# Performance work log

Measured on AMD Instinct MI355X. Metric: run time of the kernel, lower is better.

## Reference

```python
import jax, jax.numpy as jnp
import numpy as np
import math

N_HEADS = 4          # h2_dim*n_heads must equal g_dim for the stacked layers
H2_DIM = 32
G_DIM = 128
N_REL = 4
N_LAYERS = 2
PAST_W, FUT_W, PERIODIC = 5, 5, [15]
LN_EPS = 1e-5
BN_EPS = 1e-5


def _build_edges(d):
    ei, et = [], []
    for t in range(d):
        ei.append([t, t]); et.append(0)                      # self-loop
        for off in range(1, PAST_W + 1):
            if t - off >= 0:
                ei.append([t, t - off]); et.append(1)        # past
        for off in range(1, FUT_W + 1):
            if t + off < d:
                ei.append([t, t + off]); et.append(2)        # future
        for off in PERIODIC:
            if t + off < d:
                ei.append([t, t + off]); et.append(3)        # periodic fwd
            if t - off >= 0:
                ei.append([t, t - off]); et.append(3)        # periodic bwd
    return np.array(ei, dtype=np.int64).T, np.array(et, dtype=np.int64)


def setup_inputs() -> dict:
    key = jax.random.key(0)
    b, d, h, w, c = 4, 2048, 8, 8, 192
    ks = jax.random.split(key, 24)
    s = 0.05
    ei, et = _build_edges(d)
    inp = {
        'x': jax.random.normal(ks[0], (b, d, h, w, c), dtype=jnp.float32),
        'edge_index': jnp.asarray(ei),
        'edge_type': jnp.asarray(et),
        'fe_fc_w': jax.random.normal(ks[1], (c, G_DIM), dtype=jnp.float32) * s,
        'fe_fc_b': jnp.zeros((G_DIM,), jnp.float32),
        'fe_ln_g': jnp.ones((G_DIM,), jnp.float32),
        'fe_ln_b': jnp.zeros((G_DIM,), jnp.float32),
        'w_rel': jax.random.normal(ks[2], (N_LAYERS, N_REL, G_DIM, G_DIM), dtype=jnp.float32) * s,
        'w_root': jax.random.normal(ks[3], (N_LAYERS, G_DIM, G_DIM), dtype=jnp.float32) * s,
        'rgcn_b': jnp.zeros((N_LAYERS, G_DIM), jnp.float32),
        'wq': jax.random.normal(ks[4], (N_LAYERS, G_DIM, N_HEADS * H2_DIM), dtype=jnp.float32) * s,
        'bq': jnp.zeros((N_LAYERS, N_HEADS * H2_DIM), jnp.float32),
        'wk': jax.random.normal(ks[5], (N_LAYERS, G_DIM, N_HEADS * H2_DIM), dtype=jnp.float32) * s,
        'bk': jnp.zeros((N_LAYERS, N_HEADS * H2_DIM), jnp.float32),
        'wv': jax.random.normal(ks[6], (N_LAYERS, G_DIM, N_HEADS * H2_DIM), dtype=jnp.float32) * s,
        'bv': jnp.zeros((N_LAYERS, N_HEADS * H2_DIM), jnp.float32),
        'wskip': jax.random.normal(ks[7], (N_LAYERS, G_DIM, N_HEADS * H2_DIM), dtype=jnp.float32) * s,
        'bskip': jnp.zeros((N_LAYERS, N_HEADS * H2_DIM), jnp.float32),
        'bn_g': jnp.ones((N_LAYERS, N_HEADS * H2_DIM), jnp.float32),
        'bn_b': jnp.zeros((N_LAYERS, N_HEADS * H2_DIM), jnp.float32),
    }
    return inp


def _forward(x, edge_index, edge_type, fe_fc_w, fe_fc_b, fe_ln_g, fe_ln_b,
             w_rel, w_root, rgcn_b, wq, bq, wk, bk, wv, bv, wskip, bskip, bn_g, bn_b):
    d = x.shape[1]
    src, dst = edge_index[0], edge_index[1]
    rel_masks = [(edge_type == r).astype(jnp.float32) for r in range(N_REL)]
    inv_sqrt_c = 1.0 / math.sqrt(H2_DIM)

    def graph_fwd(xi):  # xi: [d,h,w,c]
        feat = xi.mean(axis=(1, 2))                         # adaptive avg pool -> [d,c]
        hfe = feat @ fe_fc_w + fe_fc_b                      # [d,g]
        mu = hfe.mean(-1, keepdims=True)
        var = ((hfe - mu) ** 2).mean(-1, keepdims=True)
        nf = (hfe - mu) / jnp.sqrt(var + LN_EPS) * fe_ln_g + fe_ln_b

        for l in range(N_LAYERS):
            # ---- RGCNConv (mean aggregation per relation + root) ----
            out = nf @ w_root[l] + rgcn_b[l]
            for r in range(N_REL):
                m = rel_masks[r]
                xr = nf @ w_rel[l, r]                       # [d,g]
                msg = xr[src] * m[:, None]                  # [E,g]
                s = jax.ops.segment_sum(msg, dst, num_segments=d)
                cnt = jax.ops.segment_sum(m, dst, num_segments=d)
                out = out + s / jnp.maximum(cnt, 1.0)[:, None]
            nf1 = out
            # ---- TransformerConv (per-head edge attention) ----
            q = (nf1 @ wq[l] + bq[l]).reshape(d, N_HEADS, H2_DIM)
            k = (nf1 @ wk[l] + bk[l]).reshape(d, N_HEADS, H2_DIM)
            v = (nf1 @ wv[l] + bv[l]).reshape(d, N_HEADS, H2_DIM)
            logits = (q[dst] * k[src]).sum(-1) * inv_sqrt_c  # [E,H]
            mx = jax.ops.segment_max(logits, dst, num_segments=d)
            a = jnp.exp(logits - mx[dst])
            denom = jax.ops.segment_sum(a, dst, num_segments=d)
            alpha = a / denom[dst]                           # softmax over incoming edges
            agg = jax.ops.segment_sum(alpha[:, :, None] * v[src], dst, num_segments=d)
            out2 = agg.reshape(d, N_HEADS * H2_DIM) + nf1 @ wskip[l] + bskip[l]
            # ---- BatchNorm1d (training-mode batch stats over nodes) ----
            bmu = out2.mean(0)
            bvar = ((out2 - bmu) ** 2).mean(0)
            out2 = (out2 - bmu) / jnp.sqrt(bvar + BN_EPS) * bn_g[l] + bn_b[l]
            nf = jax.nn.leaky_relu(out2, 0.01)
        return nf

    return jax.vmap(graph_fwd)(x)                           # [b,d,g]


def reference(x, edge_index, edge_type, fe_fc_w, fe_fc_b, fe_ln_g, fe_ln_b,
              w_rel, w_root, rgcn_b, wq, bq, wk, bk, wv, bv, wskip, bskip, bn_g, bn_b):
    return _forward(x, edge_index, edge_type, fe_fc_w, fe_fc_b, fe_ln_g, fe_ln_b,
                    w_rel, w_root, rgcn_b, wq, bq, wk, bk, wv, bv, wskip, bskip, bn_g, bn_b)
```

## Files before the change

### kernel.cpp

```cpp
#include <hip/hip_runtime.h>
#include <hip/hip_bf16.h>

#define B_ 4
#define D_ 2048
#define HWS 64
#define C_ 192
#define G_ 128
#define NODES (B_*D_)
#define R_ 16
#define HALO_ROWS 48

typedef short bf8_t  __attribute__((ext_vector_type(8)));
typedef float f32x4_t __attribute__((ext_vector_type(4)));
typedef unsigned short us4_t __attribute__((ext_vector_type(4)));

__device__ inline unsigned short f2bf(float f) {
    unsigned int u = __builtin_bit_cast(unsigned int, f);
    unsigned int r = (u + 0x7fffu + ((u >> 16) & 1u)) >> 16;
    return (unsigned short)r;
}
__device__ inline float bf2f(unsigned short h) {
    unsigned int u = ((unsigned int)h) << 16;
    return __builtin_bit_cast(float, u);
}

struct WconvArgs {
    const float* src[16];
    const float* add[16];
};
__global__ __launch_bounds__(256) void wconv_kernel(WconvArgs a, unsigned short* __restrict__ dst)
{
    int m = blockIdx.y;
    int idx = blockIdx.x * 256 + threadIdx.x;
    int n = idx >> 7;
    int k = idx & 127;
    float v = a.src[m][k * G_ + n];
    if (a.add[m]) v += a.add[m][k * G_ + n];
    dst[(size_t)m * 16384 + idx] = f2bf(v);
}

__global__ __launch_bounds__(192) void pool_fc_ln_kernel(
    const float* __restrict__ x, const float* __restrict__ W,
    const float* __restrict__ bias, const float* __restrict__ gam,
    const float* __restrict__ bet, unsigned short* __restrict__ nf)
{
    int u = blockIdx.x;
    int tid = threadIdx.x;
    __shared__ float feat[C_];
    __shared__ float4 red4[4][48];
    __shared__ float red[4];
    __shared__ float stats[2];

    const float4* xb4 = (const float4*)(x + (size_t)u * (HWS * C_));
    int cg = tid % 48;
    int rg = tid / 48;
    float4 a = make_float4(0.f, 0.f, 0.f, 0.f);
    #pragma unroll
    for (int s = 0; s < HWS; s += 4) {
        float4 v = xb4[(size_t)(s + rg) * 48 + cg];
        a.x += v.x; a.y += v.y; a.z += v.z; a.w += v.w;
    }
    red4[rg][cg] = a;
    __syncthreads();
    if (rg == 0) {
        float4 b0 = red4[0][cg], b1 = red4[1][cg], b2 = red4[2][cg], b3 = red4[3][cg];
        feat[cg * 4 + 0] = (b0.x + b1.x + b2.x + b3.x) * (1.0f / HWS);
        feat[cg * 4 + 1] = (b0.y + b1.y + b2.y + b3.y) * (1.0f / HWS);
        feat[cg * 4 + 2] = (b0.z + b1.z + b2.z + b3.z) * (1.0f / HWS);
        feat[cg * 4 + 3] = (b0.w + b1.w + b2.w + b3.w) * (1.0f / HWS);
    }
    __syncthreads();

    float h = 0.f;
    if (tid < G_) {
        h = bias[tid];
        #pragma unroll 4
        for (int c = 0; c < C_; ++c) h += feat[c] * W[c * G_ + tid];
    }
    float s1 = (tid < G_) ? h : 0.f;
    float s2 = (tid < G_) ? h * h : 0.f;
    #pragma unroll
    for (int off = 32; off >= 1; off >>= 1) {
        s1 += __shfl_xor(s1, off, 64);
        s2 += __shfl_xor(s2, off, 64);
    }
    int wid = tid >> 6;
    if ((tid & 63) == 0 && wid < 2) { red[wid] = s1; red[2 + wid] = s2; }
    __syncthreads();
    if (tid == 0) {
        float S = red[0] + red[1];
        float SS = red[2] + red[3];
        float mu = S / G_;
        float var = SS / G_ - mu * mu;
        stats[0] = mu;
        stats[1] = 1.0f / sqrtf(var + 1e-5f);
    }
    __syncthreads();
    if (tid < G_) {
        float v = (h - stats[0]) * stats[1] * gam[tid] + bet[tid];
        nf[(size_t)u * G_ + tid] = f2bf(v);
    }
}

template <bool BNIN>
__global__ __launch_bounds__(256) void rgcn_fused_kernel(
    const unsigned short* __restrict__ nf, const float* __restrict__ xin,
    const float* __restrict__ partials, const float* __restrict__ gam,
    const float* __restrict__ bet,
    const unsigned short* __restrict__ wt,
    const float* __restrict__ rb,
    unsigned short* __restrict__ out)
{
    __shared__ char raw[HALO_ROWS * 256];
    __shared__ char agg[R_ * 1024];
    __shared__ float smu[G_], sivg[G_], sbet[G_];
    __shared__ float sred[2][G_], ssred[2][G_];
    int blk = blockIdx.x;
    int b = blk >> 7;
    int t0 = (blk & 127) * R_;
    int tid = threadIdx.x;

    if constexpr (BNIN) {
        int halfk = tid >> 7;
        int c = tid & 127;
        float s = 0.f, ss = 0.f;
        const float* P = partials + (size_t)b * 128 * 256;
        #pragma unroll 4
        for (int k = halfk * 64; k < halfk * 64 + 64; ++k) {
            s += P[k * 256 + c];
            ss += P[k * 256 + G_ + c];
        }
        sred[halfk][c] = s;
        ssred[halfk][c] = ss;
        __syncthreads();
        if (tid < G_) {
            float S = sred[0][tid] + sred[1][tid];
            float SS = ssred[0][tid] + ssred[1][tid];
            float mu = S / D_;
            float var = SS / D_ - mu * mu;
            float inv = 1.0f / sqrtf(var + 1e-5f);
            smu[tid] = mu;
            sivg[tid] = inv * gam[tid];
            sbet[tid] = bet[tid];
        }
        __syncthreads();
        const float* xb = xin + (size_t)b * D_ * G_;
        #pragma unroll
        for (int p = 0; p < 3; ++p) {
            int task = tid + p * 256;
            int i = task >> 4, c16 = task & 15;
            int t = t0 - 15 + i;
            bf8_t v8 = {0, 0, 0, 0, 0, 0, 0, 0};
            if (t >= 0 && t < D_) {
                const float* vp = xb + (size_t)t * G_ + c16 * 8;
                #pragma unroll
                for (int e = 0; e < 8; ++e) {
                    int c = c16 * 8 + e;
                    float y = (vp[e] - smu[c]) * sivg[c] + sbet[c];
                    y = (y > 0.f) ? y : 0.01f * y;
                    v8[e] = (short)f2bf(y);
                }
            }
            *(bf8_t*)(raw + ((i * 256 + c16 * 16) ^ ((i & 7) << 4))) = v8;
        }
    } else {
        const unsigned short* src = nf + (size_t)b * D_ * G_;
        #pragma unroll
        for (int p = 0; p < 3; ++p) {
            int task = tid + p * 256;
            int i = task >> 4, c16 = task & 15;
            int t = t0 - 15 + i;
            bf8_t v = {0, 0, 0, 0, 0, 0, 0, 0};
            if (t >= 0 && t < D_) v = *(const bf8_t*)(src + (size_t)t * G_ + c16 * 8);
            *(bf8_t*)(raw + ((i * 256 + c16 * 16) ^ ((i & 7) << 4))) = v;
        }
    }
    __syncthreads();

    #pragma unroll
    for (int p = 0; p < 4; ++p) {
        int task = tid + p * 256;
        int c16 = task & 15, rel = (task >> 4) & 3, row = task >> 6;
        int t = t0 + row;
        int ctr = row + 15;
        float s[8] = {0.f,0.f,0.f,0.f,0.f,0.f,0.f,0.f};
        float scale = 1.f;
        if (rel == 0) {
            bf8_t v = *(const bf8_t*)(raw + ((ctr * 256 + c16 * 16) ^ ((ctr & 7) << 4)));
            #pragma unroll
            for (int e = 0; e < 8; ++e) s[e] = bf2f((unsigned short)v[e]);
        } else if (rel == 1) {
            #pragma unroll
            for (int o = 1; o <= 5; ++o) if (t + o < D_) {
                int i = ctr + o;
                bf8_t v = *(const bf8_t*)(raw + ((i * 256 + c16 * 16) ^ ((i & 7) << 4)));
                #pragma unroll
                for (int e = 0; e < 8; ++e) s[e] += bf2f((unsigned short)v[e]);
            }
            scale = 1.f / (float)max(min(5, D_ - 1 - t), 1);
        } else if (rel == 2) {
            #pragma unroll
            for (int o = 1; o <= 5; ++o) if (t - o >= 0) {
                int i = ctr - o;
                bf8_t v = *(const bf8_t*)(raw + ((i * 256 + c16 * 16) ^ ((i & 7) << 4)));
                #pragma unroll
                for (int e = 0; e < 8; ++e) s[e] += bf2f((unsigned short)v[e]);
            }
            scale = 1.f / (float)max(min(5, t), 1);
        } else {
            int cnt = 0;
            if (t >= 15) {
                int i = ctr - 15;
                bf8_t v = *(const bf8_t*)(raw + ((i * 256 + c16 * 16) ^ ((i & 7) << 4)));
                #pragma unroll
                for (int e = 0; e < 8; ++e) s[e] += bf2f((unsigned short)v[e]);
                cnt++;
            }
            if (t + 15 < D_) {
                int i = ctr + 15;
                bf8_t v = *(const bf8_t*)(raw + ((i * 256 + c16 * 16) ^ ((i & 7) << 4)));
                #pragma unroll
                for (int e = 0; e < 8; ++e) s[e] += bf2f((unsigned short)v[e]);
                cnt++;
            }
            scale = 1.f / (float)max(cnt, 1);
        }
        bf8_t o8;
        #pragma unroll
        for (int e = 0; e < 8; ++e) o8[e] = (short)f2bf(s[e] * scale);
        *(bf8_t*)(agg + ((row * 1024 + rel * 256 + c16 * 16) ^ ((row & 7) << 4))) = o8;
    }
    __syncthreads();

    int l = tid & 63, wv = tid >> 6;
    int l15 = l & 15, kgrp = l >> 4;
    int col16 = blockIdx.y * 4 + wv;
    f32x4_t acc = (f32x4_t){0.f, 0.f, 0.f, 0.f};

    for (int ks = 0; ks < 16; ++ks) {
        int rel = ks >> 2, kk = ks & 3;
        bf8_t a = *(const bf8_t*)(agg +
            ((l15 * 1024 + rel * 256 + kk * 64 + kgrp * 16) ^ ((l15 & 7) << 4)));
        bf8_t bf = *(const bf8_t*)(wt + rel * 16384 +
            (size_t)(col16 * 16 + l15) * G_ + kk * 32 + kgrp * 8);
        acc = __builtin_amdgcn_mfma_f32_16x16x32_bf16(a, bf, acc, 0, 0, 0);
    }

    unsigned short* outb = out + (size_t)b * D_ * G_;
    int rbase = t0 + kgrp * 4;
    int col = col16 * 16 + l15;
    float rbv = rb[col];
    #pragma unroll
    for (int j = 0; j < 4; ++j)
        outb[(size_t)(rbase + j) * G_ + col] = f2bf(acc[j] + rbv);
}

__device__ inline void stage_halo48(const unsigned short* __restrict__ src,
                                    int t0, char* raw, int tid)
{
    #pragma unroll
    for (int p = 0; p < 3; ++p) {
        int task = tid + p * 256;
        int i = task >> 4, c16 = task & 15;
        int t = t0 - 15 + i;
        bf8_t v = {0, 0, 0, 0, 0, 0, 0, 0};
        if (t >= 0 && t < D_) v = *(const bf8_t*)(src + (size_t)t * G_ + c16 * 8);
        *(bf8_t*)(raw + ((i * 256 + c16 * 16) ^ ((i & 7) << 4))) = v;
    }
}

__global__ __launch_bounds__(256) void qkvs_attn_kernel(
    const unsigned short* __restrict__ nf1,
    const unsigned short* __restrict__ wt,
    const float* __restrict__ bq, const float* __restrict__ bk,
    const float* __restrict__ bv, const float* __restrict__ bsk,
    float* __restrict__ out2, float* __restrict__ partials)
{
    __shared__ char raw[HALO_ROWS * 256];
    __shared__ unsigned short kls[HALO_ROWS * 64];
    __shared__ unsigned short vls[HALO_ROWS * 64];
    __shared__ unsigned short qls[R_ * 64];
    __shared__ float sls[R_ * 64];
    int blk = blockIdx.x, tid = threadIdx.x;
    int b = blk >> 7, t0 = (blk & 127) * R_;
    int y = blockIdx.y;

    stage_halo48(nf1 + (size_t)b * D_ * G_, t0, raw, tid);
    __syncthreads();

    int l = tid & 63, wvid = tid >> 6;
    int l15 = l & 15, kgrp = l >> 4;
    #pragma unroll
    for (int i = 0; i < 2; ++i) {
        int job = wvid + i * 4;
        int m, frag;
        if (job < 3)      { m = 1; frag = job; }
        else if (job < 6) { m = 2; frag = job - 3; }
        else if (job == 6){ m = 0; frag = 0; }
        else              { m = 3; frag = 0; }
        bool halo = (m == 1) | (m == 2);
        int rawrow = halo ? (frag * 16 + l15) : (15 + l15);
        const unsigned short* wm = wt + (size_t)m * 16384;
        const float* bias = (m == 0) ? bq : (m == 1) ? bk : (m == 2) ? bv : bsk;

        bf8_t a[4];
        #pragma unroll
        for (int kc = 0; kc < 4; ++kc)
            a[kc] = *(const bf8_t*)(raw +
                ((rawrow * 256 + kc * 64 + kgrp * 16) ^ ((rawrow & 7) << 4)));
        f32x4_t acc[4];
        #pragma unroll
        for (int n = 0; n < 4; ++n) acc[n] = (f32x4_t){0.f, 0.f, 0.f, 0.f};
        #pragma unroll
        for (int kc = 0; kc < 4; ++kc) {
            #pragma unroll
            for (int n = 0; n < 4; ++n) {
                int col = y * 64 + n * 16 + l15;
                bf8_t bf = *(const bf8_t*)(wm +
                    (size_t)col * G_ + kc * 32 + kgrp * 8);
                acc[n] = __builtin_amdgcn_mfma_f32_16x16x32_bf16(a[kc], bf, acc[n], 0, 0, 0);
            }
        }
        int r0 = frag * 16 + kgrp * 4;
        #pragma unroll
        for (int n = 0; n < 4; ++n) {
            int ln = n * 16 + l15;
            float bb = bias[y * 64 + ln];
            #pragma unroll
            for (int j = 0; j < 4; ++j) {
                float v = acc[n][j] + bb;
                int rr = r0 + j;
                if (m == 1)      kls[rr * 64 + ln] = f2bf(v);
                else if (m == 2) vls[rr * 64 + ln] = f2bf(v);
                else if (m == 0) qls[rr * 64 + ln] = f2bf(v);
                else             sls[rr * 64 + ln] = v;
            }
        }
    }
    __syncthreads();

    int j = tid & 63, quarter = tid >> 6;
    const float invs = 0.17677669529663687f;
    float ps = 0.f, pss = 0.f;
    float* o2b = out2 + (size_t)b * D_ * G_;
    const int offs[13] = {0, 1, 2, 3, 4, 5, -1, -2, -3, -4, -5, -15, 15};
    for (int it = 0; it < 4; ++it) {
        int tl = it * 4 + quarter;
        int t = t0 + tl;
        float q = bf2f(qls[tl * 64 + j]);
        float lg[13], vv[13];
        #pragma unroll
        for (int n = 0; n < 13; ++n) {
            int ts = t + offs[n];
            bool ok = (ts >= 0) && (ts < D_);
            int ki = tl + 15 + offs[n];
            float kk = ok ? bf2f(kls[ki * 64 + j]) : 0.f;
            vv[n] = ok ? bf2f(vls[ki * 64 + j]) : 0.f;
            float p = q * kk;
            p += __shfl_xor(p, 16, 32);
            p += __shfl_xor(p, 8, 32);
            p += __shfl_xor(p, 4, 32);
            p += __shfl_xor(p, 2, 32);
            p += __shfl_xor(p, 1, 32);
            lg[n] = ok ? p * invs : -1e30f;
        }
        float m = lg[0];
        #pragma unroll
        for (int n = 1; n < 13; ++n) m = fmaxf(m, lg[n]);
        float den = 0.f, aggv = 0.f;
        #pragma unroll
        for (int n = 0; n < 13; ++n) {
            float e = expf(lg[n] - m);
            den += e;
            aggv += e * vv[n];
        }
        float o = aggv / den + sls[tl * 64 + j];
        o2b[(size_t)t * G_ + y * 64 + j] = o;
        ps += o; pss += o * o;
    }

    __syncthreads();
    float* red = (float*)raw;
    red[quarter * 64 + j] = ps;
    red[256 + quarter * 64 + j] = pss;
    __syncthreads();
    if (tid < 64) {
        float s = 0.f, ss = 0.f;
        #pragma unroll
        for (int qq = 0; qq < 4; ++qq) {
            s += red[qq * 64 + tid];
            ss += red[256 + qq * 64 + tid];
        }
        float* P = partials + ((size_t)b * 128 + (blk & 127)) * 256;
        P[y * 64 + tid] = s;
        P[128 + y * 64 + tid] = ss;
    }
}

__global__ __launch_bounds__(256) void bn_apply_kernel(
    const float* __restrict__ X, const float* __restrict__ partials,
    const float* __restrict__ gam, const float* __restrict__ bet,
    float* __restrict__ out)
{
    int chunk = blockIdx.x;
    int b = blockIdx.y;
    int tid = threadIdx.x;
    __shared__ float smu[G_], sinv[G_];
    if (tid < G_) {
        float s = 0.f, ss = 0.f;
        const float* P = partials + (size_t)b * 128 * 256;
        #pragma unroll 4
        for (int k = 0; k < 128; ++k) {
            s += P[k * 256 + tid];
            ss += P[k * 256 + G_ + tid];
        }
        float mu = s / D_;
        float var = ss / D_ - mu * mu;
        smu[tid] = mu;
        sinv[tid] = 1.0f / sqrtf(var + 1e-5f);
    }
    __syncthreads();

    const float4* base4 = (const float4*)(X + ((size_t)b * D_ + chunk * 64) * G_);
    int c4 = (tid & 31) * 4;
    float m0 = smu[c4], m1 = smu[c4 + 1], m2 = smu[c4 + 2], m3 = smu[c4 + 3];
    float i0 = sinv[c4] * gam[c4],     i1 = sinv[c4 + 1] * gam[c4 + 1];
    float i2 = sinv[c4 + 2] * gam[c4 + 2], i3 = sinv[c4 + 3] * gam[c4 + 3];
    float b0 = bet[c4], b1 = bet[c4 + 1], b2 = bet[c4 + 2], b3 = bet[c4 + 3];
    #pragma unroll
    for (int p = 0; p < 8; ++p) {
        float4 v = base4[p * 256 + tid];
        float4 y;
        y.x = (v.x - m0) * i0 + b0;
        y.y = (v.y - m1) * i1 + b1;
        y.z = (v.z - m2) * i2 + b2;
        y.w = (v.w - m3) * i3 + b3;
        y.x = (y.x > 0.f) ? y.x : 0.01f * y.x;
        y.y = (y.y > 0.f) ? y.y : 0.01f * y.y;
        y.z = (y.z > 0.f) ? y.z : 0.01f * y.z;
        y.w = (y.w > 0.f) ? y.w : 0.01f * y.w;
        float4* ob = (float4*)(out + ((size_t)b * D_ + chunk * 64) * G_);
        ob[p * 256 + tid] = y;
    }
}

extern "C" void kernel_launch(void* const* d_in, const int* in_sizes, int n_in,
                              void* d_out, int out_size, void* d_ws, size_t ws_size,
                              hipStream_t stream)
{
    (void)in_sizes; (void)n_in; (void)out_size; (void)ws_size;
    const float* x      = (const float*)d_in[0];
    const float* fe_w   = (const float*)d_in[3];
    const float* fe_b   = (const float*)d_in[4];
    const float* ln_g   = (const float*)d_in[5];
    const float* ln_b   = (const float*)d_in[6];
    const float* w_rel  = (const float*)d_in[7];
    const float* w_root = (const float*)d_in[8];
    const float* rgcn_b = (const float*)d_in[9];
    const float* wq  = (const float*)d_in[10];
    const float* bq  = (const float*)d_in[11];
    const float* wk  = (const float*)d_in[12];
    const float* bk  = (const float*)d_in[13];
    const float* wv  = (const float*)d_in[14];
    const float* bv  = (const float*)d_in[15];
    const float* wsk = (const float*)d_in[16];
    const float* bsk = (const float*)d_in[17];
    const float* bn_g = (const float*)d_in[18];
    const float* bn_b = (const float*)d_in[19];

    float* ws   = (float*)d_ws;
    float* out2 = ws;
    float* partials = out2 + (size_t)NODES * G_;
    unsigned short* nf_bf  = (unsigned short*)(partials + 4 * 128 * 256);
    unsigned short* nf1_bf = nf_bf + (size_t)NODES * G_;
    unsigned short* wbf    = nf1_bf + (size_t)NODES * G_;

    WconvArgs wa;
    for (int l = 0; l < 2; ++l) {
        for (int r = 0; r < 4; ++r) {
            wa.src[l * 8 + r] = w_rel + ((size_t)l * 4 + r) * G_ * G_;
            wa.add[l * 8 + r] = (r == 0) ? (w_root + (size_t)l * G_ * G_) : nullptr;
        }
        wa.src[l * 8 + 4] = wq  + (size_t)l * G_ * G_; wa.add[l * 8 + 4] = nullptr;
        wa.src[l * 8 + 5] = wk  + (size_t)l * G_ * G_; wa.add[l * 8 + 5] = nullptr;
        wa.src[l * 8 + 6] = wv  + (size_t)l * G_ * G_; wa.add[l * 8 + 6] = nullptr;
        wa.src[l * 8 + 7] = wsk + (size_t)l * G_ * G_; wa.add[l * 8 + 7] = nullptr;
    }
    wconv_kernel<<<dim3(64, 16), 256, 0, stream>>>(wa, wbf);

    pool_fc_ln_kernel<<<NODES, 192, 0, stream>>>(x, fe_w, fe_b, ln_g, ln_b, nf_bf);

    rgcn_fused_kernel<false><<<dim3(512, 2), 256, 0, stream>>>(
        nf_bf, nullptr, nullptr, nullptr, nullptr,
        wbf, rgcn_b, nf1_bf);
    qkvs_attn_kernel<<<dim3(512, 2), 256, 0, stream>>>(
        nf1_bf, wbf + (size_t)4 * 16384,
        bq, bk, bv, bsk, out2, partials);

    rgcn_fused_kernel<true><<<dim3(512, 2), 256, 0, stream>>>(
        nullptr, out2, partials, bn_g, bn_b,
        wbf + (size_t)8 * 16384, rgcn_b + G_, nf1_bf);
    qkvs_attn_kernel<<<dim3(512, 2), 256, 0, stream>>>(
        nf1_bf, wbf + (size_t)12 * 16384,
        bq + G_, bk + G_, bv + G_, bsk + G_, out2, partials);

    bn_apply_kernel<<<dim3(32, 4), 256, 0, stream>>>(
        out2, partials, bn_g + G_, bn_b + G_, (float*)d_out);
}
```

Before: 225.6 us.

## Fuse RGCN, attention and BN phases into one persistent kernel with grid barriers

Replaces the four per-layer kernels and the final BN-apply kernel with a single persistent kernel of 512 blocks, separated by atomic-counter grid barriers. Each block now processes both column halves serially instead of using a second grid dimension, and shared memory is unioned across phases. This removes kernel launch gaps and tail effects between dependent stages. It adds barrier spin costs, requires all blocks to be co-resident, halves the block count per phase, and relies on a timeout-bounded spin that could break ordering if blocks are not resident.

```diff
diff --git a/kernel.cpp b/kernel.cpp
--- a/kernel.cpp
+++ b/kernel.cpp
@@ -9,6 +9,7 @@
 #define NODES (B_*D_)
 #define R_ 16
 #define HALO_ROWS 48
+#define NBLK 512
 
 typedef short bf8_t  __attribute__((ext_vector_type(8)));
 typedef float f32x4_t __attribute__((ext_vector_type(4)));
@@ -22,6 +23,23 @@
 __device__ inline float bf2f(unsigned short h) {
     unsigned int u = ((unsigned int)h) << 16;
     return __builtin_bit_cast(float, u);
+}
+
+__device__ inline void gbar(unsigned* cnt, int tid)
+{
+    __syncthreads();
+    __threadfence();
+    if (tid == 0) {
+        __hip_atomic_fetch_add(cnt, 1u, __ATOMIC_ACQ_REL, __HIP_MEMORY_SCOPE_AGENT);
+        long it = 0;
+        while (__hip_atomic_load(cnt, __ATOMIC_ACQUIRE, __HIP_MEMORY_SCOPE_AGENT) < NBLK
+               && it < (1L << 22)) {
+            __builtin_amdgcn_s_sleep(8);
+            ++it;
+        }
+    }
+    __syncthreads();
+    __threadfence();
 }
 
 struct WconvArgs {
@@ -102,23 +120,39 @@
     }
 }
 
+struct ShR {
+    char raw[HALO_ROWS * 256];
+    char agg[R_ * 1024];
+    float smu[G_], sivg[G_], sbet[G_];
+    float sred[2][G_], ssred[2][G_];
+};
+struct ShQ {
+    char raw[HALO_ROWS * 256];
+    unsigned short kls[HALO_ROWS * 64];
+    unsigned short vls[HALO_ROWS * 64];
+    unsigned short qls[R_ * 64];
+    float sls[R_ * 64];
+    float redsc[512];
+};
+struct ShB {
+    float smu[G_], sinv[G_];
+    float sred[2][G_], ssred[2][G_];
+};
+union ShU { ShR r; ShQ q; ShB b; };
+
 template <bool BNIN>
-__global__ __launch_bounds__(256) void rgcn_fused_kernel(
+__device__ __forceinline__ void rgcn_phase(
+    ShR& sh,
     const unsigned short* __restrict__ nf, const float* __restrict__ xin,
     const float* __restrict__ partials, const float* __restrict__ gam,
     const float* __restrict__ bet,
-    const unsigned short* __restrict__ wt,
-    const float* __restrict__ rb,
-    unsigned short* __restrict__ out)
-{
-    __shared__ char raw[HALO_ROWS * 256];
-    __shared__ char agg[R_ * 1024];
-    __shared__ float smu[G_], sivg[G_], sbet[G_];
-    __shared__ float sred[2][G_], ssred[2][G_];
-    int blk = blockIdx.x;
+    const unsigned short* __restrict__ wt, const float* __restrict__ rb,
+    unsigned short* __restrict__ out, int blk, int tid)
+{
+    char* raw = sh.raw;
+    char* agg = sh.agg;
     int b = blk >> 7;
     int t0 = (blk & 127) * R_;
-    int tid = threadIdx.x;
 
     if constexpr (BNIN) {
         int halfk = tid >> 7;
@@ -130,18 +164,18 @@
             s += P[k * 256 + c];
             ss += P[k * 256 + G_ + c];
         }
-        sred[halfk][c] = s;
-        ssred[halfk][c] = ss;
+        sh.sred[halfk][c] = s;
+        sh.ssred[halfk][c] = ss;
         __syncthreads();
         if (tid < G_) {
-            float S = sred[0][tid] + sred[1][tid];
-            float SS = ssred[0][tid] + ssred[1][tid];
+            float S = sh.sred[0][tid] + sh.sred[1][tid];
+            float SS = sh.ssred[0][tid] + sh.ssred[1][tid];
             float mu = S / D_;
             float var = SS / D_ - mu * mu;
             float inv = 1.0f / sqrtf(var + 1e-5f);
-            smu[tid] = mu;
-            sivg[tid] = inv * gam[tid];
-            sbet[tid] = bet[tid];
+            sh.smu[tid] = mu;
+            sh.sivg[tid] = inv * gam[tid];
+            sh.sbet[tid] = bet[tid];
         }
         __syncthreads();
         const float* xb = xin + (size_t)b * D_ * G_;
@@ -156,9 +190,9 @@
                 #pragma unroll
                 for (int e = 0; e < 8; ++e) {
                     int c = c16 * 8 + e;
-                    float y = (vp[e] - smu[c]) * sivg[c] + sbet[c];
-                    y = (y > 0.f) ? y : 0.01f * y;
-                    v8[e] = (short)f2bf(y);
+                    float yv = (vp[e] - sh.smu[c]) * sh.sivg[c] + sh.sbet[c];
+                    yv = (yv > 0.f) ? yv : 0.01f * yv;
+                    v8[e] = (short)f2bf(yv);
                 }
             }
             *(bf8_t*)(raw + ((i * 256 + c16 * 16) ^ ((i & 7) << 4))) = v8;
@@ -234,201 +268,208 @@
 
     int l = tid & 63, wv = tid >> 6;
     int l15 = l & 15, kgrp = l >> 4;
-    int col16 = blockIdx.y * 4 + wv;
-    f32x4_t acc = (f32x4_t){0.f, 0.f, 0.f, 0.f};
-
-    for (int ks = 0; ks < 16; ++ks) {
-        int rel = ks >> 2, kk = ks & 3;
-        bf8_t a = *(const bf8_t*)(agg +
-            ((l15 * 1024 + rel * 256 + kk * 64 + kgrp * 16) ^ ((l15 & 7) << 4)));
-        bf8_t bf = *(const bf8_t*)(wt + rel * 16384 +
-            (size_t)(col16 * 16 + l15) * G_ + kk * 32 + kgrp * 8);
-        acc = __builtin_amdgcn_mfma_f32_16x16x32_bf16(a, bf, acc, 0, 0, 0);
-    }
-
     unsigned short* outb = out + (size_t)b * D_ * G_;
     int rbase = t0 + kgrp * 4;
-    int col = col16 * 16 + l15;
-    float rbv = rb[col];
+
     #pragma unroll
-    for (int j = 0; j < 4; ++j)
-        outb[(size_t)(rbase + j) * G_ + col] = f2bf(acc[j] + rbv);
-}
-
-__device__ inline void stage_halo48(const unsigned short* __restrict__ src,
-                                    int t0, char* raw, int tid)
-{
-    #pragma unroll
-    for (int p = 0; p < 3; ++p) {
-        int task = tid + p * 256;
-        int i = task >> 4, c16 = task & 15;
-        int t = t0 - 15 + i;
-        bf8_t v = {0, 0, 0, 0, 0, 0, 0, 0};
-        if (t >= 0 && t < D_) v = *(const bf8_t*)(src + (size_t)t * G_ + c16 * 8);
-        *(bf8_t*)(raw + ((i * 256 + c16 * 16) ^ ((i & 7) << 4))) = v;
-    }
-}
-
-__global__ __launch_bounds__(256) void qkvs_attn_kernel(
+    for (int y = 0; y < 2; ++y) {
+        int col16 = y * 4 + wv;
+        f32x4_t acc = (f32x4_t){0.f, 0.f, 0.f, 0.f};
+        for (int ks = 0; ks < 16; ++ks) {
+            int rel = ks >> 2, kk = ks & 3;
+            bf8_t a = *(const bf8_t*)(agg +
+                ((l15 * 1024 + rel * 256 + kk * 64 + kgrp * 16) ^ ((l15 & 7) << 4)));
+            bf8_t bf = *(const bf8_t*)(wt + rel * 16384 +
+                (size_t)(col16 * 16 + l15) * G_ + kk * 32 + kgrp * 8);
+            acc = __builtin_amdgcn_mfma_f32_16x16x32_bf16(a, bf, acc, 0, 0, 0);
+        }
+        int col = col16 * 16 + l15;
+        float rbv = rb[col];
+        #pragma unroll
+        for (int j = 0; j < 4; ++j)
+            outb[(size_t)(rbase + j) * G_ + col] = f2bf(acc[j] + rbv);
+    }
+}
+
+__device__ __forceinline__ void qkvs_phase(
+    ShQ& sh,
     const unsigned short* __restrict__ nf1,
     const unsigned short* __restrict__ wt,
     const float* __restrict__ bq, const float* __restrict__ bk,
     const float* __restrict__ bv, const float* __restrict__ bsk,
-    float* __restrict__ out2, float* __restrict__ partials)
-{
-    __shared__ char raw[HALO_ROWS * 256];
-    __shared__ unsigned short kls[HALO_ROWS * 64];
-    __shared__ unsigned short vls[HALO_ROWS * 64];
-    __shared__ unsigned short qls[R_ * 64];
-    __shared__ float sls[R_ * 64];
-    int blk = blockIdx.x, tid = threadIdx.x;
+    float* __restrict__ out2, float* __restrict__ partials,
+    int blk, int tid)
+{
+    char* raw = sh.raw;
     int b = blk >> 7, t0 = (blk & 127) * R_;
-    int y = blockIdx.y;
-
-    stage_halo48(nf1 + (size_t)b * D_ * G_, t0, raw, tid);
+
+    {
+        const unsigned short* src = nf1 + (size_t)b * D_ * G_;
+        #pragma unroll
+        for (int p = 0; p < 3; ++p) {
+            int task = tid + p * 256;
+            int i = task >> 4, c16 = task & 15;
+            int t = t0 - 15 + i;
+            bf8_t v = {0, 0, 0, 0, 0, 0, 0, 0};
+            if (t >= 0 && t < D_) v = *(const bf8_t*)(src + (size_t)t * G_ + c16 * 8);
+            *(bf8_t*)(raw + ((i * 256 + c16 * 16) ^ ((i & 7) << 4))) = v;
+        }
+    }
     __syncthreads();
 
     int l = tid & 63, wvid = tid >> 6;
     int l15 = l & 15, kgrp = l >> 4;
-    #pragma unroll
-    for (int i = 0; i < 2; ++i) {
-        int job = wvid + i * 4;
-        int m, frag;
-        if (job < 3)      { m = 1; frag = job; }
-        else if (job < 6) { m = 2; frag = job - 3; }
-        else if (job == 6){ m = 0; frag = 0; }
-        else              { m = 3; frag = 0; }
-        bool halo = (m == 1) | (m == 2);
-        int rawrow = halo ? (frag * 16 + l15) : (15 + l15);
-        const unsigned short* wm = wt + (size_t)m * 16384;
-        const float* bias = (m == 0) ? bq : (m == 1) ? bk : (m == 2) ? bv : bsk;
-
-        bf8_t a[4];
+    const float invs = 0.17677669529663687f;
+    const int offs[13] = {0, 1, 2, 3, 4, 5, -1, -2, -3, -4, -5, -15, 15};
+    float* o2b = out2 + (size_t)b * D_ * G_;
+
+    for (int y = 0; y < 2; ++y) {
         #pragma unroll
-        for (int kc = 0; kc < 4; ++kc)
-            a[kc] = *(const bf8_t*)(raw +
-                ((rawrow * 256 + kc * 64 + kgrp * 16) ^ ((rawrow & 7) << 4)));
-        f32x4_t acc[4];
-        #pragma unroll
-        for (int n = 0; n < 4; ++n) acc[n] = (f32x4_t){0.f, 0.f, 0.f, 0.f};
-        #pragma unroll
-        for (int kc = 0; kc < 4; ++kc) {
+        for (int i = 0; i < 2; ++i) {
+            int job = wvid + i * 4;
+            int m, frag;
+            if (job < 3)      { m = 1; frag = job; }
+            else if (job < 6) { m = 2; frag = job - 3; }
+            else if (job == 6){ m = 0; frag = 0; }
+            else              { m = 3; frag = 0; }
+            bool halo = (m == 1) | (m == 2);
+            int rawrow = halo ? (frag * 16 + l15) : (15 + l15);
+            const unsigned short* wm = wt + (size_t)m * 16384;
+            const float* bias = (m == 0) ? bq : (m == 1) ? bk : (m == 2) ? bv : bsk;
+
+            bf8_t a[4];
+            #pragma unroll
+            for (int kc = 0; kc < 4; ++kc)
+                a[kc] = *(const bf8_t*)(raw +
+                    ((rawrow * 256 + kc * 64 + kgrp * 16) ^ ((rawrow & 7) << 4)));
+            f32x4_t acc[4];
+            #pragma unroll
+            for (int n = 0; n < 4; ++n) acc[n] = (f32x4_t){0.f, 0.f, 0.f, 0.f};
+            #pragma unroll
+            for (int kc = 0; kc < 4; ++kc) {
+                #pragma unroll
+                for (int n = 0; n < 4; ++n) {
+                    int col = y * 64 + n * 16 + l15;
+                    bf8_t bf = *(const bf8_t*)(wm +
+                        (size_t)col * G_ + kc * 32 + kgrp * 8);
+                    acc[n] = __builtin_amdgcn_mfma_f32_16x16x32_bf16(a[kc], bf, acc[n], 0, 0, 0);
+                }
+            }
+            int r0 = frag * 16 + kgrp * 4;
             #pragma unroll
             for (int n = 0; n < 4; ++n) {
-                int col = y * 64 + n * 16 + l15;
-                bf8_t bf = *(const bf8_t*)(wm +
-                    (size_t)col * G_ + kc * 32 + kgrp * 8);
-                acc[n] = __builtin_amdgcn_mfma_f32_16x16x32_bf16(a[kc], bf, acc[n], 0, 0, 0);
-            }
-        }
-        int r0 = frag * 16 + kgrp * 4;
-        #pragma unroll
-        for (int n = 0; n < 4; ++n) {
-            int ln = n * 16 + l15;
-            float bb = bias[y * 64 + ln];
-            #pragma unroll
-            for (int j = 0; j < 4; ++j) {
-                float v = acc[n][j] + bb;
-                int rr = r0 + j;
-                if (m == 1)      kls[rr * 64 + ln] = f2bf(v);
-                else if (m == 2) vls[rr * 64 + ln] = f2bf(v);
-                else if (m == 0) qls[rr * 64 + ln] = f2bf(v);
-                else             sls[rr * 64 + ln] = v;
-            }
-        }
-    }
-    __syncthreads();
-
-    int j = tid & 63, quarter = tid >> 6;
-    const float invs = 0.17677669529663687f;
-    float ps = 0.f, pss = 0.f;
-    float* o2b = out2 + (size_t)b * D_ * G_;
-    const int offs[13] = {0, 1, 2, 3, 4, 5, -1, -2, -3, -4, -5, -15, 15};
-    for (int it = 0; it < 4; ++it) {
-        int tl = it * 4 + quarter;
-        int t = t0 + tl;
-        float q = bf2f(qls[tl * 64 + j]);
-        float lg[13], vv[13];
-        #pragma unroll
-        for (int n = 0; n < 13; ++n) {
-            int ts = t + offs[n];
-            bool ok = (ts >= 0) && (ts < D_);
-            int ki = tl + 15 + offs[n];
-            float kk = ok ? bf2f(kls[ki * 64 + j]) : 0.f;
-            vv[n] = ok ? bf2f(vls[ki * 64 + j]) : 0.f;
-            float p = q * kk;
-            p += __shfl_xor(p, 16, 32);
-            p += __shfl_xor(p, 8, 32);
-            p += __shfl_xor(p, 4, 32);
-            p += __shfl_xor(p, 2, 32);
-            p += __shfl_xor(p, 1, 32);
-            lg[n] = ok ? p * invs : -1e30f;
-        }
-        float m = lg[0];
-        #pragma unroll
-        for (int n = 1; n < 13; ++n) m = fmaxf(m, lg[n]);
-        float den = 0.f, aggv = 0.f;
-        #pragma unroll
-        for (int n = 0; n < 13; ++n) {
-            float e = expf(lg[n] - m);
-            den += e;
-            aggv += e * vv[n];
-        }
-        float o = aggv / den + sls[tl * 64 + j];
-        o2b[(size_t)t * G_ + y * 64 + j] = o;
-        ps += o; pss += o * o;
-    }
-
-    __syncthreads();
-    float* red = (float*)raw;
-    red[quarter * 64 + j] = ps;
-    red[256 + quarter * 64 + j] = pss;
-    __syncthreads();
-    if (tid < 64) {
-        float s = 0.f, ss = 0.f;
-        #pragma unroll
-        for (int qq = 0; qq < 4; ++qq) {
-            s += red[qq * 64 + tid];
-            ss += red[256 + qq * 64 + tid];
-        }
-        float* P = partials + ((size_t)b * 128 + (blk & 127)) * 256;
-        P[y * 64 + tid] = s;
-        P[128 + y * 64 + tid] = ss;
-    }
-}
-
-__global__ __launch_bounds__(256) void bn_apply_kernel(
+                int ln = n * 16 + l15;
+                float bb = bias[y * 64 + ln];
+                #pragma unroll
+                for (int j = 0; j < 4; ++j) {
+                    float v = acc[n][j] + bb;
+                    int rr = r0 + j;
+                    if (m == 1)      sh.kls[rr * 64 + ln] = f2bf(v);
+                    else if (m == 2) sh.vls[rr * 64 + ln] = f2bf(v);
+                    else if (m == 0) sh.qls[rr * 64 + ln] = f2bf(v);
+                    else             sh.sls[rr * 64 + ln] = v;
+                }
+            }
+        }
+        __syncthreads();
+
+        int j = tid & 63, quarter = tid >> 6;
+        float ps = 0.f, pss = 0.f;
+        for (int it = 0; it < 4; ++it) {
+            int tl = it * 4 + quarter;
+            int t = t0 + tl;
+            float q = bf2f(sh.qls[tl * 64 + j]);
+            float lg[13], vv[13];
+            #pragma unroll
+            for (int n = 0; n < 13; ++n) {
+                int ts = t + offs[n];
+                bool ok = (ts >= 0) && (ts < D_);
+                int ki = tl + 15 + offs[n];
+                float kk = ok ? bf2f(sh.kls[ki * 64 + j]) : 0.f;
+                vv[n] = ok ? bf2f(sh.vls[ki * 64 + j]) : 0.f;
+                float p = q * kk;
+                p += __shfl_xor(p, 16, 32);
+                p += __shfl_xor(p, 8, 32);
+                p += __shfl_xor(p, 4, 32);
+                p += __shfl_xor(p, 2, 32);
+                p += __shfl_xor(p, 1, 32);
+                lg[n] = ok ? p * invs : -1e30f;
+            }
+            float m = lg[0];
+            #pragma unroll
+            for (int n = 1; n < 13; ++n) m = fmaxf(m, lg[n]);
+            float den = 0.f, aggv = 0.f;
+            #pragma unroll
+            for (int n = 0; n < 13; ++n) {
+                float e = expf(lg[n] - m);
+                den += e;
+                aggv += e * vv[n];
+            }
+            float o = aggv / den + sh.sls[tl * 64 + j];
+            o2b[(size_t)t * G_ + y * 64 + j] = o;
+            ps += o; pss += o * o;
+        }
+        __syncthreads();
+
+        sh.redsc[quarter * 64 + j] = ps;
+        sh.redsc[256 + quarter * 64 + j] = pss;
+        __syncthreads();
+        if (tid < 64) {
+            float s = 0.f, ss = 0.f;
+            #pragma unroll
+            for (int qq = 0; qq < 4; ++qq) {
+                s += sh.redsc[qq * 64 + tid];
+                ss += sh.redsc[256 + qq * 64 + tid];
+            }
+            float* P = partials + ((size_t)b * 128 + (blk & 127)) * 256;
+            P[y * 64 + tid] = s;
+            P[128 + y * 64 + tid] = ss;
+        }
+        __syncthreads();
+    }
+}
+
+__device__ __forceinline__ void bn_final_phase(
+    ShB& sh,
     const float* __restrict__ X, const float* __restrict__ partials,
     const float* __restrict__ gam, const float* __restrict__ bet,
-    float* __restrict__ out)
-{
-    int chunk = blockIdx.x;
-    int b = blockIdx.y;
-    int tid = threadIdx.x;
-    __shared__ float smu[G_], sinv[G_];
-    if (tid < G_) {
+    float* __restrict__ out, int blk, int tid)
+{
+    int b = blk >> 7;
+    int chunk = blk & 127;
+    {
+        int halfk = tid >> 7;
+        int c = tid & 127;
         float s = 0.f, ss = 0.f;
         const float* P = partials + (size_t)b * 128 * 256;
         #pragma unroll 4
-        for (int k = 0; k < 128; ++k) {
-            s += P[k * 256 + tid];
-            ss += P[k * 256 + G_ + tid];
-        }
-        float mu = s / D_;
-        float var = ss / D_ - mu * mu;
-        smu[tid] = mu;
-        sinv[tid] = 1.0f / sqrtf(var + 1e-5f);
-    }
-    __syncthreads();
-
-    const float4* base4 = (const float4*)(X + ((size_t)b * D_ + chunk * 64) * G_);
+        for (int k = halfk * 64; k < halfk * 64 + 64; ++k) {
+            s += P[k * 256 + c];
+            ss += P[k * 256 + G_ + c];
+        }
+        sh.sred[halfk][c] = s;
+        sh.ssred[halfk][c] = ss;
+    }
+    __syncthreads();
+    if (tid < G_) {
+        float S = sh.sred[0][tid] + sh.sred[1][tid];
+        float SS = sh.ssred[0][tid] + sh.ssred[1][tid];
+        float mu = S / D_;
+        float var = SS / D_ - mu * mu;
+        sh.smu[tid] = mu;
+        sh.sinv[tid] = 1.0f / sqrtf(var + 1e-5f);
+    }
+    __syncthreads();
+
+    const float4* base4 = (const float4*)(X + ((size_t)b * D_ + chunk * 16) * G_);
+    float4* ob4 = (float4*)(out + ((size_t)b * D_ + chunk * 16) * G_);
     int c4 = (tid & 31) * 4;
-    float m0 = smu[c4], m1 = smu[c4 + 1], m2 = smu[c4 + 2], m3 = smu[c4 + 3];
-    float i0 = sinv[c4] * gam[c4],     i1 = sinv[c4 + 1] * gam[c4 + 1];
-    float i2 = sinv[c4 + 2] * gam[c4 + 2], i3 = sinv[c4 + 3] * gam[c4 + 3];
+    float m0 = sh.smu[c4], m1 = sh.smu[c4 + 1], m2 = sh.smu[c4 + 2], m3 = sh.smu[c4 + 3];
+    float i0 = sh.sinv[c4] * gam[c4],     i1 = sh.sinv[c4 + 1] * gam[c4 + 1];
+    float i2 = sh.sinv[c4 + 2] * gam[c4 + 2], i3 = sh.sinv[c4 + 3] * gam[c4 + 3];
     float b0 = bet[c4], b1 = bet[c4 + 1], b2 = bet[c4 + 2], b3 = bet[c4 + 3];
     #pragma unroll
-    for (int p = 0; p < 8; ++p) {
+    for (int p = 0; p < 2; ++p) {
         float4 v = base4[p * 256 + tid];
         float4 y;
         y.x = (v.x - m0) * i0 + b0;
@@ -439,9 +480,48 @@
         y.y = (y.y > 0.f) ? y.y : 0.01f * y.y;
         y.z = (y.z > 0.f) ? y.z : 0.01f * y.z;
         y.w = (y.w > 0.f) ? y.w : 0.01f * y.w;
-        float4* ob = (float4*)(out + ((size_t)b * D_ + chunk * 64) * G_);
-        ob[p * 256 + tid] = y;
-    }
+        ob4[p * 256 + tid] = y;
+    }
+}
+
+struct MegaArgs {
+    const unsigned short* nf;
+    unsigned short* nf1;
+    float* out2;
+    float* partials;
+    const unsigned short* wbf;
+    const float* rgcn_b;
+    const float* bq; const float* bk; const float* bv; const float* bsk;
+    const float* bn_g; const float* bn_b;
+    float* dout;
+    unsigned* counters;
+};
+
+__global__ __launch_bounds__(256, 2) void mega_kernel(MegaArgs a)
+{
+    __shared__ ShU sh;
+    int blk = blockIdx.x;
+    int tid = threadIdx.x;
+
+    rgcn_phase<false>(sh.r, a.nf, nullptr, nullptr, nullptr, nullptr,
+                      a.wbf, a.rgcn_b, a.nf1, blk, tid);
+    gbar(a.counters + 0, tid);
+
+    qkvs_phase(sh.q, a.nf1, a.wbf + (size_t)4 * 16384,
+               a.bq, a.bk, a.bv, a.bsk, a.out2, a.partials, blk, tid);
+    gbar(a.counters + 1, tid);
+
+    rgcn_phase<true>(sh.r, nullptr, a.out2, a.partials, a.bn_g, a.bn_b,
+                     a.wbf + (size_t)8 * 16384, a.rgcn_b + G_, a.nf1, blk, tid);
+    gbar(a.counters + 2, tid);
+
+    qkvs_phase(sh.q, a.nf1, a.wbf + (size_t)12 * 16384,
+               a.bq + G_, a.bk + G_, a.bv + G_, a.bsk + G_,
+               a.out2, a.partials, blk, tid);
+    gbar(a.counters + 3, tid);
+
+    bn_final_phase(sh.b, a.out2, a.partials, a.bn_g + G_, a.bn_b + G_,
+                   a.dout, blk, tid);
 }
 
 extern "C" void kernel_launch(void* const* d_in, const int* in_sizes, int n_in,
@@ -474,6 +554,9 @@
     unsigned short* nf_bf  = (unsigned short*)(partials + 4 * 128 * 256);
     unsigned short* nf1_bf = nf_bf + (size_t)NODES * G_;
     unsigned short* wbf    = nf1_bf + (size_t)NODES * G_;
+    unsigned* counters     = (unsigned*)(wbf + (size_t)16 * 16384);
+
+    hipMemsetAsync(counters, 0, 4 * sizeof(unsigned), stream);
 
     WconvArgs wa;
     for (int l = 0; l < 2; ++l) {
@@ -490,20 +573,11 @@
 
     pool_fc_ln_kernel<<<NODES, 192, 0, stream>>>(x, fe_w, fe_b, ln_g, ln_b, nf_bf);
 
-    rgcn_fused_kernel<false><<<dim3(512, 2), 256, 0, stream>>>(
-        nf_bf, nullptr, nullptr, nullptr, nullptr,
-        wbf, rgcn_b, nf1_bf);
-    qkvs_attn_kernel<<<dim3(512, 2), 256, 0, stream>>>(
-        nf1_bf, wbf + (size_t)4 * 16384,
-        bq, bk, bv, bsk, out2, partials);
-
-    rgcn_fused_kernel<true><<<dim3(512, 2), 256, 0, stream>>>(
-        nullptr, out2, partials, bn_g, bn_b,
-        wbf + (size_t)8 * 16384, rgcn_b + G_, nf1_bf);
-    qkvs_attn_kernel<<<dim3(512, 2), 256, 0, stream>>>(
-        nf1_bf, wbf + (size_t)12 * 16384,
-        bq + G_, bk + G_, bv + G_, bsk + G_, out2, partials);
-
-    bn_apply_kernel<<<dim3(32, 4), 256, 0, stream>>>(
-        out2, partials, bn_g + G_, bn_b + G_, (float*)d_out);
-}
+    MegaArgs ma;
+    ma.nf = nf_bf; ma.nf1 = nf1_bf; ma.out2 = out2; ma.partials = partials;
+    ma.wbf = wbf; ma.rgcn_b = rgcn_b;
+    ma.bq = bq; ma.bk = bk; ma.bv = bv; ma.bsk = bsk;
+    ma.bn_g = bn_g; ma.bn_b = bn_b; ma.dout = (float*)d_out;
+    ma.counters = counters;
+    mega_kernel<<<NBLK, 256, 0, stream>>>(ma);
+}
```

Result: slower. 627.1 us (+177.9%).
